# Performance work log

Measured on AMD Instinct MI355X. Metric: run time of the kernel, lower is better.

Reference implementation:

```python
import jax, jax.numpy as jnp
import numpy as np

N, D = 16384, 4096  # anchors x candidates


def setup_inputs() -> dict:
    key = jax.random.key(0)
    k1, k2 = jax.random.split(key)
    labels = jax.random.normal(k1, (N, D), dtype=jnp.float32)
    logits = jax.random.normal(k2, (N, D), dtype=jnp.float32)
    mask = jnp.ones((N, D), dtype=jnp.bool_)  # accepted by the torch module but unused
    alpha = jnp.full((1,), 0.07, dtype=jnp.float32)  # temperature
    return {"labels": labels, "logits": logits, "mask": mask, "alpha": alpha}


def reference(labels, logits, mask, alpha):
    # logits / alpha, then cross-entropy against the argmax-of-labels column.
    # The torch code's masked_select + concat merely moves the positive column
    # to index 0 before CE with target 0 -- mathematically identical to this.
    scaled = logits / alpha  # [N, D]
    pos_idx = jnp.argmax(labels, axis=1)  # [N]
    logz = jax.nn.logsumexp(scaled, axis=1)  # [N], stable
    pos = jnp.take_along_axis(scaled, pos_idx[:, None], axis=1)[:, 0]  # [N]
    return jnp.mean(logz - pos)
```

## Files before the change

kernel.cpp:

```cpp
#include <hip/hip_runtime.h>
#include <math.h>


typedef float vf4 __attribute__((ext_vector_type(4)));

constexpr int Dk    = 4096;
constexpr int BLOCK = 256;
constexpr int ROWS_PER_BLOCK = 4;

__global__ __launch_bounds__(BLOCK) void nce_main(
    const float* __restrict__ labels, const float* __restrict__ logits,
    const float* __restrict__ alpha, float* __restrict__ bins)
{
    const int lane = threadIdx.x & 63;
    const int wave = threadIdx.x >> 6;
    const int row  = blockIdx.x * ROWS_PER_BLOCK + wave;
    const size_t base = (size_t)row * Dk;
    const vf4* g4 = reinterpret_cast<const vf4*>(logits + base);
    const vf4* l4 = reinterpret_cast<const vf4*>(labels + base);
    const float ia = 1.0f / alpha[0];

    float m = -INFINITY, s = 0.0f;
    float lmax = -INFINITY, lval = 0.0f;
    int   lidx = 0x7fffffff;

#pragma unroll 1
    for (int half = 0; half < 2; ++half) {
        const int c0 = half * 8;
        vf4 g[8], l[8];
#pragma unroll
        for (int j = 0; j < 8; ++j)
            g[j] = __builtin_nontemporal_load(g4 + lane + 64 * (c0 + j));
#pragma unroll
        for (int j = 0; j < 8; ++j)
            l[j] = __builtin_nontemporal_load(l4 + lane + 64 * (c0 + j));

#pragma unroll
        for (int j = 0; j < 8; ++j) {
            const float c4 = fmaxf(fmaxf(g[j][0], g[j][1]), fmaxf(g[j][2], g[j][3]));
            const float mn = fmaxf(m, c4);
            const float e0 = __expf((g[j][0] - mn) * ia);
            const float e1 = __expf((g[j][1] - mn) * ia);
            const float e2 = __expf((g[j][2] - mn) * ia);
            const float e3 = __expf((g[j][3] - mn) * ia);
            s = s * __expf((m - mn) * ia) + ((e0 + e1) + (e2 + e3));
            m = mn;
#pragma unroll
            for (int e = 0; e < 4; ++e) {
                const float le  = l[j][e];
                const int   idx = 4 * (lane + 64 * (c0 + j)) + e;
                if (le > lmax || (le == lmax && idx < lidx)) {
                    lmax = le; lidx = idx; lval = g[j][e];
                }
            }
        }
    }

    float M = m;
#pragma unroll
    for (int off = 1; off < 64; off <<= 1)
        M = fmaxf(M, __shfl_xor(M, off));
    s *= __expf((m - M) * ia);

#pragma unroll
    for (int off = 32; off; off >>= 1) {
        s += __shfl_down(s, off);
        const float om = __shfl_down(lmax, off);
        const int   oi = __shfl_down(lidx, off);
        const float ov = __shfl_down(lval, off);
        if (om > lmax || (om == lmax && oi < lidx)) { lmax = om; lidx = oi; lval = ov; }
    }

    if (lane == 0)
        bins[row] = (M - lval) * ia + logf(s);
}

__global__ __launch_bounds__(BLOCK) void nce_finalize(
    const float* __restrict__ bins, float* __restrict__ out, int n, float inv_n)
{
    const int t = threadIdx.x;
    float v = 0.0f;
    for (int i = t; i < n; i += BLOCK) v += bins[i];
#pragma unroll
    for (int off = 32; off; off >>= 1) v += __shfl_down(v, off);
    __shared__ float s_w[BLOCK / 64];
    if ((t & 63) == 0) s_w[t >> 6] = v;
    __syncthreads();
    if (t == 0) out[0] = (s_w[0] + s_w[1] + s_w[2] + s_w[3]) * inv_n;
}

extern "C" void kernel_launch(void* const* d_in, const int* in_sizes, int n_in,
                              void* d_out, int out_size, void* d_ws, size_t ws_size,
                              hipStream_t stream) {
    const float* labels = (const float*)d_in[0];
    const float* logits = (const float*)d_in[1];
    const float* alpha  = (const float*)d_in[3];
    float* out  = (float*)d_out;
    float* bins = (float*)d_ws;

    const int N = in_sizes[0] / Dk;

    nce_main<<<N / ROWS_PER_BLOCK, BLOCK, 0, stream>>>(labels, logits, alpha, bins);
    nce_finalize<<<1, BLOCK, 0, stream>>>(bins, out, N, 1.0f / (float)N);
}
```

Before: 589.6 us.

## Hold full logits row in registers and double-buffer label loads

Loads all 16 logit vectors per lane up front and streams labels through a two-slot register double buffer while the argmax scan runs. Replaces the online max-rescaled exp sum with a two-pass scheme: a tree max over the registers plus a wave reduction, then a plain exp sum with four independent accumulators. This removes the serial rescale dependency chain and keeps more loads in flight. It raises register pressure (64 floats of logits plus label buffers), which may lower occupancy.

```diff
diff --git a/kernel.cpp b/kernel.cpp
--- a/kernel.cpp
+++ b/kernel.cpp
@@ -6,61 +6,84 @@
 
 constexpr int Dk    = 4096;
 constexpr int BLOCK = 256;
-constexpr int ROWS_PER_BLOCK = 4;
+constexpr int RPB   = 4;
 
 __global__ __launch_bounds__(BLOCK) void nce_main(
     const float* __restrict__ labels, const float* __restrict__ logits,
     const float* __restrict__ alpha, float* __restrict__ bins)
 {
     const int lane = threadIdx.x & 63;
-    const int wave = threadIdx.x >> 6;
-    const int row  = blockIdx.x * ROWS_PER_BLOCK + wave;
+    const int row  = blockIdx.x * RPB + (threadIdx.x >> 6);
     const size_t base = (size_t)row * Dk;
     const vf4* g4 = reinterpret_cast<const vf4*>(logits + base);
     const vf4* l4 = reinterpret_cast<const vf4*>(labels + base);
     const float ia = 1.0f / alpha[0];
 
-    float m = -INFINITY, s = 0.0f;
+    vf4 g[16];
+#pragma unroll
+    for (int j = 0; j < 16; ++j)
+        g[j] = __builtin_nontemporal_load(g4 + lane + 64 * j);
+
+    vf4 lb[2][4];
+#pragma unroll
+    for (int j = 0; j < 4; ++j)
+        lb[0][j] = __builtin_nontemporal_load(l4 + lane + 64 * j);
+#pragma unroll
+    for (int j = 0; j < 4; ++j)
+        lb[1][j] = __builtin_nontemporal_load(l4 + lane + 64 * (4 + j));
+
     float lmax = -INFINITY, lval = 0.0f;
     int   lidx = 0x7fffffff;
 
-#pragma unroll 1
-    for (int half = 0; half < 2; ++half) {
-        const int c0 = half * 8;
-        vf4 g[8], l[8];
 #pragma unroll
-        for (int j = 0; j < 8; ++j)
-            g[j] = __builtin_nontemporal_load(g4 + lane + 64 * (c0 + j));
+    for (int c = 0; c < 4; ++c) {
+        const int b = c & 1;
 #pragma unroll
-        for (int j = 0; j < 8; ++j)
-            l[j] = __builtin_nontemporal_load(l4 + lane + 64 * (c0 + j));
-
-#pragma unroll
-        for (int j = 0; j < 8; ++j) {
-            const float c4 = fmaxf(fmaxf(g[j][0], g[j][1]), fmaxf(g[j][2], g[j][3]));
-            const float mn = fmaxf(m, c4);
-            const float e0 = __expf((g[j][0] - mn) * ia);
-            const float e1 = __expf((g[j][1] - mn) * ia);
-            const float e2 = __expf((g[j][2] - mn) * ia);
-            const float e3 = __expf((g[j][3] - mn) * ia);
-            s = s * __expf((m - mn) * ia) + ((e0 + e1) + (e2 + e3));
-            m = mn;
+        for (int j = 0; j < 4; ++j) {
+            const int jj = 4 * c + j;
 #pragma unroll
             for (int e = 0; e < 4; ++e) {
-                const float le  = l[j][e];
-                const int   idx = 4 * (lane + 64 * (c0 + j)) + e;
+                const float le  = lb[b][j][e];
+                const int   idx = 4 * (lane + 64 * jj) + e;
                 if (le > lmax || (le == lmax && idx < lidx)) {
-                    lmax = le; lidx = idx; lval = g[j][e];
+                    lmax = le; lidx = idx; lval = g[jj][e];
                 }
             }
         }
+        if (c + 2 < 4) {
+#pragma unroll
+            for (int j = 0; j < 4; ++j)
+                lb[b][j] = __builtin_nontemporal_load(l4 + lane + 64 * (4 * (c + 2) + j));
+        }
     }
 
-    float M = m;
+    float pm[16];
+#pragma unroll
+    for (int j = 0; j < 16; ++j)
+        pm[j] = fmaxf(fmaxf(g[j][0], g[j][1]), fmaxf(g[j][2], g[j][3]));
+#pragma unroll
+    for (int off = 8; off; off >>= 1)
+#pragma unroll
+        for (int j = 0; j < 16; ++j)
+            if (j < off) pm[j] = fmaxf(pm[j], pm[j + off]);
+    float M = pm[0];
 #pragma unroll
     for (int off = 1; off < 64; off <<= 1)
         M = fmaxf(M, __shfl_xor(M, off));
-    s *= __expf((m - M) * ia);
+
+    float s0 = 0.f, s1 = 0.f, s2 = 0.f, s3 = 0.f;
+#pragma unroll
+    for (int j = 0; j < 16; j += 4) {
+        s0 += __expf((g[j+0][0] - M) * ia) + __expf((g[j+0][1] - M) * ia)
+            + __expf((g[j+0][2] - M) * ia) + __expf((g[j+0][3] - M) * ia);
+        s1 += __expf((g[j+1][0] - M) * ia) + __expf((g[j+1][1] - M) * ia)
+            + __expf((g[j+1][2] - M) * ia) + __expf((g[j+1][3] - M) * ia);
+        s2 += __expf((g[j+2][0] - M) * ia) + __expf((g[j+2][1] - M) * ia)
+            + __expf((g[j+2][2] - M) * ia) + __expf((g[j+2][3] - M) * ia);
+        s3 += __expf((g[j+3][0] - M) * ia) + __expf((g[j+3][1] - M) * ia)
+            + __expf((g[j+3][2] - M) * ia) + __expf((g[j+3][3] - M) * ia);
+    }
+    float s = (s0 + s1) + (s2 + s3);
 
 #pragma unroll
     for (int off = 32; off; off >>= 1) {
@@ -100,6 +123,6 @@
 
     const int N = in_sizes[0] / Dk;
 
-    nce_main<<<N / ROWS_PER_BLOCK, BLOCK, 0, stream>>>(labels, logits, alpha, bins);
+    nce_main<<<N / RPB, BLOCK, 0, stream>>>(labels, logits, alpha, bins);
     nce_finalize<<<1, BLOCK, 0, stream>>>(bins, out, N, 1.0f / (float)N);
 }
```

Result: no change. 592.4 us (+0.5%).
